# Optimization experiments

Measured on AMD Instinct MI355X. Metric: run time of the kernel, lower is better.

The kernel has to match this reference:

```python
import jax, jax.numpy as jnp
import numpy as np

B, N = 8, 512
EMBED, EDGE_D, FLAG_D = 256, 32, 32
NODE_NUM, EDGE_NUM, FLAG_NUM = 20000, 16, 4
IN_DIM = 2 * EMBED + 2 * FLAG_D + EDGE_D  # concat order: [head_emb, tail_emb, head_flag, tail_flag, edge]
NEG = -1e12


def setup_inputs() -> dict:
    key = jax.random.key(0)
    ks = jax.random.split(key, 16)
    s = 0.05
    return {
        "adjacent_matrix": jax.random.randint(ks[0], (B, N, N), 0, 2, dtype=jnp.int32),
        "head_nodes": jax.random.randint(ks[1], (B, N), 0, NODE_NUM, dtype=jnp.int32),
        "head_flag_bit_matrix": jax.random.randint(ks[2], (B, N), 0, FLAG_NUM, dtype=jnp.int32),
        "edge_type_matrix": jax.random.randint(ks[3], (B, N, N), 0, EDGE_NUM, dtype=jnp.int32),
        "node_emb": jax.random.normal(ks[4], (NODE_NUM, EMBED)) * s,
        "edge_emb": jax.random.normal(ks[5], (EDGE_NUM, EDGE_D)) * s,
        "flag_emb": jax.random.normal(ks[6], (FLAG_NUM, FLAG_D)) * s,
        "t1_w": jax.random.normal(ks[7], (EMBED, EMBED)) * s,
        "t1_b": jax.random.normal(ks[8], (EMBED,)) * s,
        "w1": jax.random.normal(ks[9], (IN_DIM,)) * s,
        "b1": jax.random.normal(ks[10], ()) * s,
        "t2_w": jax.random.normal(ks[11], (EMBED, EMBED)) * s,
        "t2_b": jax.random.normal(ks[12], (EMBED,)) * s,
        "w2": jax.random.normal(ks[13], (IN_DIM,)) * s,
        "b2": jax.random.normal(ks[14], ()) * s,
    }


def _leaky_relu(x):
    return jnp.where(x > 0, x, 0.1 * x)


def _gat_layer(h, f, e, adj, w, b):
    # Decompose Linear(concat([h_i, h_j, f_i, f_j, e_ij])) into per-part dot
    # products summed by broadcasting -> avoids the [B,N,N,IN_DIM] concat.
    D, F = h.shape[-1], f.shape[-1]
    wh, wt = w[:D], w[D:2 * D]
    wfh, wft = w[2 * D:2 * D + F], w[2 * D + F:2 * D + 2 * F]
    we = w[2 * D + 2 * F:]
    logit = ((h @ wh)[:, :, None] + (h @ wt)[:, None, :]
             + (f @ wfh)[:, :, None] + (f @ wft)[:, None, :]
             + jnp.einsum('bije,e->bij', e, we) + b)  # [B,N,N]
    logit = _leaky_relu(logit)
    logit = jnp.where(adj == 0, NEG, logit)
    att = jax.nn.softmax(logit, axis=1)  # softmax over head axis i
    # out[b,j] = sum_i att[b,i,j] * h[b,i]   (== bmm(att^T, h))
    return jnp.einsum('bij,bid->bjd', att, h)


def reference(adjacent_matrix, head_nodes, head_flag_bit_matrix, edge_type_matrix,
              node_emb, edge_emb, flag_emb,
              t1_w, t1_b, w1, b1, t2_w, t2_b, w2, b2):
    h = node_emb[head_nodes] @ t1_w.T + t1_b          # [B,N,D] (t1 projection)
    f = flag_emb[head_flag_bit_matrix]                # [B,N,F]
    e = edge_emb[edge_type_matrix]                    # [B,N,N,E]
    t = _gat_layer(h, f, e, adjacent_matrix, w1, b1)  # layer 1 aggregate
    t = jax.nn.sigmoid(t)
    h2 = t @ t2_w.T + t2_b                            # t2 projection
    return _gat_layer(h2, f, e, adjacent_matrix, w2, b2)
```

## Files before the change

### kernel.cpp

```cpp
#include <hip/hip_runtime.h>
#include <hip/hip_bf16.h>

#define BB 8
#define NN 512
#define DD 256
#define NROWS (BB*NN)
#define JT 16

using bf16x8 = __attribute__((ext_vector_type(8))) short;
using f32x4  = __attribute__((ext_vector_type(4))) float;
typedef unsigned short us_t;

__device__ __forceinline__ us_t f2bf(float x) {
    union { float f; unsigned int u; } v; v.f = x;
    unsigned int r = (v.u + 0x7fffu + ((v.u >> 16) & 1u)) >> 16;
    return (us_t)r;
}

__global__ __launch_bounds__(256) void prep_w(
    const float* __restrict__ w1f, const float* __restrict__ w2f,
    us_t* __restrict__ o1, us_t* __restrict__ o2)
{
    int i = blockIdx.x*1024 + threadIdx.x*4;
    float4 a = *(const float4*)(w1f + i);
    float4 b = *(const float4*)(w2f + i);
    ushort4 u;
    u.x = f2bf(a.x); u.y = f2bf(a.y); u.z = f2bf(a.z); u.w = f2bf(a.w);
    *(ushort4*)&o1[i] = u;
    u.x = f2bf(b.x); u.y = f2bf(b.y); u.z = f2bf(b.z); u.w = f2bf(b.w);
    *(ushort4*)&o2[i] = u;
}

__device__ __forceinline__ void lin_body(
    int bid, int t,
    const us_t* __restrict__ Wbf, const float* __restrict__ bias,
    const float* __restrict__ Xf, const int* __restrict__ idx,
    const float* __restrict__ wvec, const int* __restrict__ flagidx,
    const float* __restrict__ flag_emb,
    us_t* __restrict__ hT, float* __restrict__ aout, float* __restrict__ cout,
    float* redA, float* redC)
{
    const int wave = t >> 6, lane = t & 63;
    const int lrow = lane & 15, kg = lane >> 4;
    const int r0 = bid * 16;
    const int dw = wave * 64;

    const int arow = r0 + lrow;
    const int nid = idx ? idx[arow] : arow;

    f32x4 acc[4];
    #pragma unroll
    for (int n = 0; n < 4; ++n) acc[n] = (f32x4){0.f, 0.f, 0.f, 0.f};

    const float4* xr = (const float4*)(Xf + (size_t)nid * DD);
    #pragma unroll
    for (int ks = 0; ks < DD/32; ++ks) {
        float4 xa = xr[ks*8 + kg*2];
        float4 xb = xr[ks*8 + kg*2 + 1];
        bf16x8 af;
        af[0] = (short)f2bf(xa.x); af[1] = (short)f2bf(xa.y);
        af[2] = (short)f2bf(xa.z); af[3] = (short)f2bf(xa.w);
        af[4] = (short)f2bf(xb.x); af[5] = (short)f2bf(xb.y);
        af[6] = (short)f2bf(xb.z); af[7] = (short)f2bf(xb.w);
        #pragma unroll
        for (int n = 0; n < 4; ++n) {
            bf16x8 bfr = *(const bf16x8*)(Wbf + (size_t)(dw + n*16 + lrow)*DD
                                           + ks*32 + kg*8);
            acc[n] = __builtin_amdgcn_mfma_f32_16x16x32_bf16(af, bfr, acc[n], 0, 0, 0);
        }
    }

    const int b  = r0 >> 9;
    const int i0 = (r0 & 511) + kg*4;
    float pa[4] = {0.f,0.f,0.f,0.f}, pc[4] = {0.f,0.f,0.f,0.f};
    #pragma unroll
    for (int n = 0; n < 4; ++n) {
        int d = dw + n*16 + lrow;
        float bv = bias[d];
        float whd = wvec[d], wtd = wvec[256+d];
        ushort4 u;
        #pragma unroll
        for (int r = 0; r < 4; ++r) {
            float v = acc[n][r] + bv;
            ((us_t*)&u)[r] = f2bf(v);
            pa[r] += v * whd;
            pc[r] += v * wtd;
        }
        *(ushort4*)&hT[(size_t)b*DD*NN + (size_t)d*NN + i0] = u;
    }
    #pragma unroll
    for (int r = 0; r < 4; ++r) {
        #pragma unroll
        for (int m = 1; m < 16; m <<= 1) {
            pa[r] += __shfl_xor(pa[r], m);
            pc[r] += __shfl_xor(pc[r], m);
        }
    }
    if (lrow == 0) {
        #pragma unroll
        for (int r = 0; r < 4; ++r) {
            redA[wave*16 + kg*4 + r] = pa[r];
            redC[wave*16 + kg*4 + r] = pc[r];
        }
    }
    __syncthreads();
    if (t < 128) {
        const int m = t >> 3, sub = t & 7;
        const int fi = flagidx[r0 + m];
        float fa = 0.f, fc = 0.f;
        #pragma unroll
        for (int q = 0; q < 4; ++q) {
            int e = sub*4 + q;
            float fe = flag_emb[fi*32 + e];
            fa += fe * wvec[512 + e];
            fc += fe * wvec[544 + e];
        }
        #pragma unroll
        for (int mm = 1; mm < 8; mm <<= 1) {
            fa += __shfl_xor(fa, mm);
            fc += __shfl_xor(fc, mm);
        }
        if (sub == 0) {
            float sa = fa, sc = fc;
            #pragma unroll
            for (int wv = 0; wv < 4; ++wv) { sa += redA[wv*16 + m]; sc += redC[wv*16 + m]; }
            aout[r0 + m] = sa;
            cout[r0 + m] = sc;
        }
    }
}

__global__ __launch_bounds__(256) void k1(
    const us_t* __restrict__ Wb1, const float* __restrict__ bias1,
    const float* __restrict__ node_emb, const int* __restrict__ head_nodes,
    const float* __restrict__ wvec1, const int* __restrict__ flagidx,
    const float* __restrict__ flag_emb,
    us_t* __restrict__ hT, float* __restrict__ a1, float* __restrict__ c1,
    const int* __restrict__ adj, const int* __restrict__ et,
    unsigned char* __restrict__ pk)
{
    __shared__ float redA[64], redC[64];
    const int blk = blockIdx.x, t = threadIdx.x;
    if (blk < 256) {
        lin_body(blk, t, Wb1, bias1, node_emb, head_nodes,
                 wvec1, flagidx, flag_emb, hT, a1, c1, redA, redC);
    } else {
        int g = ((blk - 256)*256 + t)*4;
        int4 av = *(const int4*)(adj + g);
        int4 ev = *(const int4*)(et + g);
        uchar4 u;
        u.x = (unsigned char)((ev.x&15)|(av.x<<4));
        u.y = (unsigned char)((ev.y&15)|(av.y<<4));
        u.z = (unsigned char)((ev.z&15)|(av.z<<4));
        u.w = (unsigned char)((ev.w&15)|(av.w<<4));
        *(uchar4*)(pk + g) = u;
    }
}

__global__ __launch_bounds__(512) void attn1_lin2(
    const unsigned char* __restrict__ pk,
    const float* __restrict__ edge_emb, const float* __restrict__ w,
    const float* __restrict__ bptr,
    const float* __restrict__ a, const float* __restrict__ c,
    const us_t* __restrict__ hT,
    const us_t* __restrict__ Wb2, const float* __restrict__ bias2,
    const float* __restrict__ wvec2, const int* __restrict__ flagidx,
    const float* __restrict__ flag_emb,
    us_t* __restrict__ hT2, float* __restrict__ a2, float* __restrict__ c2)
{
    __shared__ __align__(16) float p[NN][JT+1];
    __shared__ __align__(16) us_t Pb[JT][NN+8];
    __shared__ __align__(16) us_t Sg[16][DD+8];
    __shared__ float as[NN];
    __shared__ float edot[16];
    __shared__ float cjs[JT];
    __shared__ float red[32][JT];
    __shared__ float mj[JT];
    __shared__ float invden[JT];

    float* redA = &red[0][0];
    float* redC = &red[8][0];

    const int t = threadIdx.x;
    const int b  = blockIdx.x >> 5;
    const int j0 = (blockIdx.x & 31) * JT;

    as[t & 511] = a[b*NN + (t & 511)];
    if (t < 16) {
        float s = 0.f;
        for (int e2 = 0; e2 < 32; ++e2)
            s += edge_emb[t*32 + e2] * w[576 + e2];
        edot[t] = s;
    } else if (t < 32) {
        cjs[t-16] = c[b*NN + j0 + (t-16)];
    }
    const float bias = bptr[0];
    __syncthreads();

    const unsigned char* pkb = pk + (size_t)b*NN*NN + j0;
    #pragma unroll
    for (int it = 0; it < 4; ++it) {
        int lid4 = (it*512 + t) * 4;
        int i = lid4 >> 4, jj = lid4 & 15;
        uchar4 u = *(const uchar4*)(pkb + (size_t)i*NN + jj);
        float base = as[i] + bias;
        unsigned char uv[4] = {u.x, u.y, u.z, u.w};
        #pragma unroll
        for (int q = 0; q < 4; ++q) {
            float l = base + cjs[jj+q] + edot[uv[q] & 15];
            l = (l > 0.f) ? l : 0.1f*l;
            p[i][jj+q] = (uv[q] >> 4) ? l : -1.0e30f;
        }
    }
    __syncthreads();

    const int j = t & 15, grp = t >> 4;
    float m = -3.0e38f;
    #pragma unroll
    for (int s = 0; s < 16; ++s) m = fmaxf(m, p[grp + s*32][j]);
    red[grp][j] = m;
    __syncthreads();
    if (t < 16) {
        float mm = red[0][t];
        for (int g2 = 1; g2 < 32; ++g2) mm = fmaxf(mm, red[g2][t]);
        mj[t] = mm;
    }
    __syncthreads();
    const float mmax = mj[j];
    float ssum = 0.f;
    #pragma unroll
    for (int s = 0; s < 16; ++s) {
        float v = __expf(p[grp + s*32][j] - mmax);
        p[grp + s*32][j] = v;
        ssum += v;
    }
    red[grp][j] = ssum;
    __syncthreads();
    if (t < 16) {
        float sm = 0.f;
        for (int g2 = 0; g2 < 32; ++g2) sm += red[g2][t];
        invden[t] = 1.f / sm;
    }
    __syncthreads();

    const float inv = invden[j];
    #pragma unroll
    for (int s = 0; s < 8; ++s) {
        int i = grp*2 + s*64;
        ushort2 u;
        u.x = f2bf(p[i  ][j] * inv);
        u.y = f2bf(p[i+1][j] * inv);
        *(ushort2*)&Pb[j][i] = u;
    }
    __syncthreads();

    const int wave = t >> 6, lane = t & 63;
    const int dw = wave * 32;
    const int lrow = lane & 15;
    const int kg   = lane >> 4;
    f32x4 acc[2];
    acc[0] = (f32x4){0.f,0.f,0.f,0.f};
    acc[1] = (f32x4){0.f,0.f,0.f,0.f};

    const us_t* hTb = hT + (size_t)b*DD*NN;
    const us_t* hp[2];
    hp[0] = hTb + (size_t)(dw + lrow)*NN + kg*8;
    hp[1] = hTb + (size_t)(dw + 16 + lrow)*NN + kg*8;

    #pragma unroll 4
    for (int ks = 0; ks < NN/32; ++ks) {
        int k0 = ks*32;
        bf16x8 afr = *(const bf16x8*)&Pb[lrow][kg*8 + k0];
        #pragma unroll
        for (int n = 0; n < 2; ++n) {
            bf16x8 bfr = *(const bf16x8*)(hp[n] + k0);
            acc[n] = __builtin_amdgcn_mfma_f32_16x16x32_bf16(afr, bfr, acc[n], 0, 0, 0);
        }
    }

    #pragma unroll
    for (int n = 0; n < 2; ++n) {
        #pragma unroll
        for (int r = 0; r < 4; ++r) {
            float v = 1.f/(1.f + __expf(-acc[n][r]));
            Sg[kg*4 + r][dw + n*16 + lrow] = f2bf(v);
        }
    }
    __syncthreads();

    f32x4 acc2[2];
    acc2[0] = (f32x4){0.f,0.f,0.f,0.f};
    acc2[1] = (f32x4){0.f,0.f,0.f,0.f};
    #pragma unroll
    for (int ks = 0; ks < DD/32; ++ks) {
        bf16x8 af2 = *(const bf16x8*)&Sg[lrow][ks*32 + kg*8];
        #pragma unroll
        for (int n = 0; n < 2; ++n) {
            bf16x8 bf2 = *(const bf16x8*)(Wb2 + (size_t)(dw + n*16 + lrow)*DD
                                           + ks*32 + kg*8);
            acc2[n] = __builtin_amdgcn_mfma_f32_16x16x32_bf16(af2, bf2, acc2[n], 0, 0, 0);
        }
    }

    const int r0 = b*NN + j0;
    const int i0 = j0 + kg*4;
    float pa[4] = {0.f,0.f,0.f,0.f}, pc[4] = {0.f,0.f,0.f,0.f};
    #pragma unroll
    for (int n = 0; n < 2; ++n) {
        int d = dw + n*16 + lrow;
        float bv = bias2[d];
        float whd = wvec2[d], wtd = wvec2[256+d];
        ushort4 u;
        #pragma unroll
        for (int r = 0; r < 4; ++r) {
            float v = acc2[n][r] + bv;
            ((us_t*)&u)[r] = f2bf(v);
            pa[r] += v * whd;
            pc[r] += v * wtd;
        }
        *(ushort4*)&hT2[(size_t)b*DD*NN + (size_t)d*NN + i0] = u;
    }
    #pragma unroll
    for (int r = 0; r < 4; ++r) {
        #pragma unroll
        for (int mk = 1; mk < 16; mk <<= 1) {
            pa[r] += __shfl_xor(pa[r], mk);
            pc[r] += __shfl_xor(pc[r], mk);
        }
    }
    __syncthreads();
    if (lrow == 0) {
        #pragma unroll
        for (int r = 0; r < 4; ++r) {
            redA[wave*16 + kg*4 + r] = pa[r];
            redC[wave*16 + kg*4 + r] = pc[r];
        }
    }
    __syncthreads();
    if (t < 128) {
        const int mrow = t >> 3, sub = t & 7;
        const int fi = flagidx[r0 + mrow];
        float fa = 0.f, fc = 0.f;
        #pragma unroll
        for (int q = 0; q < 4; ++q) {
            int e = sub*4 + q;
            float fe = flag_emb[fi*32 + e];
            fa += fe * wvec2[512 + e];
            fc += fe * wvec2[544 + e];
        }
        #pragma unroll
        for (int mm = 1; mm < 8; mm <<= 1) {
            fa += __shfl_xor(fa, mm);
            fc += __shfl_xor(fc, mm);
        }
        if (sub == 0) {
            float sa = fa, sc = fc;
            #pragma unroll
            for (int wv = 0; wv < 8; ++wv) { sa += redA[wv*16 + mrow]; sc += redC[wv*16 + mrow]; }
            a2[r0 + mrow] = sa;
            c2[r0 + mrow] = sc;
        }
    }
}

__global__ __launch_bounds__(512) void attn2(
    const unsigned char* __restrict__ pk,
    const float* __restrict__ edge_emb, const float* __restrict__ w,
    const float* __restrict__ bptr,
    const float* __restrict__ a, const float* __restrict__ c,
    const us_t* __restrict__ hT,
    float* __restrict__ outf)
{
    __shared__ __align__(16) float p[NN][JT+1];
    __shared__ __align__(16) us_t Pb[JT][NN+8];
    __shared__ float as[NN];
    __shared__ float edot[16];
    __shared__ float cjs[JT];
    __shared__ float red[32][JT];
    __shared__ float mj[JT];
    __shared__ float invden[JT];

    const int t = threadIdx.x;
    const int b  = blockIdx.x >> 5;
    const int j0 = (blockIdx.x & 31) * JT;

    as[t & 511] = a[b*NN + (t & 511)];
    if (t < 16) {
        float s = 0.f;
        for (int e2 = 0; e2 < 32; ++e2)
            s += edge_emb[t*32 + e2] * w[576 + e2];
        edot[t] = s;
    } else if (t < 32) {
        cjs[t-16] = c[b*NN + j0 + (t-16)];
    }
    const float bias = bptr[0];
    __syncthreads();

    const unsigned char* pkb = pk + (size_t)b*NN*NN + j0;
    #pragma unroll
    for (int it = 0; it < 4; ++it) {
        int lid4 = (it*512 + t) * 4;
        int i = lid4 >> 4, jj = lid4 & 15;
        uchar4 u = *(const uchar4*)(pkb + (size_t)i*NN + jj);
        float base = as[i] + bias;
        unsigned char uv[4] = {u.x, u.y, u.z, u.w};
        #pragma unroll
        for (int q = 0; q < 4; ++q) {
            float l = base + cjs[jj+q] + edot[uv[q] & 15];
            l = (l > 0.f) ? l : 0.1f*l;
            p[i][jj+q] = (uv[q] >> 4) ? l : -1.0e30f;
        }
    }
    __syncthreads();

    const int j = t & 15, grp = t >> 4;
    float m = -3.0e38f;
    #pragma unroll
    for (int s = 0; s < 16; ++s) m = fmaxf(m, p[grp + s*32][j]);
    red[grp][j] = m;
    __syncthreads();
    if (t < 16) {
        float mm = red[0][t];
        for (int g2 = 1; g2 < 32; ++g2) mm = fmaxf(mm, red[g2][t]);
        mj[t] = mm;
    }
    __syncthreads();
    const float mmax = mj[j];
    float ssum = 0.f;
    #pragma unroll
    for (int s = 0; s < 16; ++s) {
        float v = __expf(p[grp + s*32][j] - mmax);
        p[grp + s*32][j] = v;
        ssum += v;
    }
    red[grp][j] = ssum;
    __syncthreads();
    if (t < 16) {
        float sm = 0.f;
        for (int g2 = 0; g2 < 32; ++g2) sm += red[g2][t];
        invden[t] = 1.f / sm;
    }
    __syncthreads();

    const float inv = invden[j];
    #pragma unroll
    for (int s = 0; s < 8; ++s) {
        int i = grp*2 + s*64;
        ushort2 u;
        u.x = f2bf(p[i  ][j] * inv);
        u.y = f2bf(p[i+1][j] * inv);
        *(ushort2*)&Pb[j][i] = u;
    }
    __syncthreads();

    const int wave = t >> 6, lane = t & 63;
    const int dw = wave * 32;
    const int lrow = lane & 15;
    const int kg   = lane >> 4;
    f32x4 acc[2];
    acc[0] = (f32x4){0.f,0.f,0.f,0.f};
    acc[1] = (f32x4){0.f,0.f,0.f,0.f};

    const us_t* hTb = hT + (size_t)b*DD*NN;
    const us_t* hp[2];
    hp[0] = hTb + (size_t)(dw + lrow)*NN + kg*8;
    hp[1] = hTb + (size_t)(dw + 16 + lrow)*NN + kg*8;

    #pragma unroll 4
    for (int ks = 0; ks < NN/32; ++ks) {
        int k0 = ks*32;
        bf16x8 afr = *(const bf16x8*)&Pb[lrow][kg*8 + k0];
        #pragma unroll
        for (int n = 0; n < 2; ++n) {
            bf16x8 bfr = *(const bf16x8*)(hp[n] + k0);
            acc[n] = __builtin_amdgcn_mfma_f32_16x16x32_bf16(afr, bfr, acc[n], 0, 0, 0);
        }
    }

    #pragma unroll
    for (int n = 0; n < 2; ++n) {
        #pragma unroll
        for (int r = 0; r < 4; ++r) {
            int jj = j0 + kg*4 + r;
            int dd = dw + n*16 + lrow;
            outf[(size_t)(b*NN + jj)*DD + dd] = acc[n][r];
        }
    }
}

extern "C" void kernel_launch(void* const* d_in, const int* in_sizes, int n_in,
                              void* d_out, int out_size, void* d_ws, size_t ws_size,
                              hipStream_t stream) {
    (void)in_sizes; (void)n_in; (void)out_size; (void)ws_size;
    const int*   adj       = (const int*)d_in[0];
    const int*   head_nodes= (const int*)d_in[1];
    const int*   head_flag = (const int*)d_in[2];
    const int*   etype     = (const int*)d_in[3];
    const float* node_emb  = (const float*)d_in[4];
    const float* edge_emb  = (const float*)d_in[5];
    const float* flag_emb  = (const float*)d_in[6];
    const float* t1_w      = (const float*)d_in[7];
    const float* t1_b      = (const float*)d_in[8];
    const float* w1        = (const float*)d_in[9];
    const float* b1        = (const float*)d_in[10];
    const float* t2_w      = (const float*)d_in[11];
    const float* t2_b      = (const float*)d_in[12];
    const float* w2        = (const float*)d_in[13];
    const float* b2        = (const float*)d_in[14];

    us_t* hT1 = (us_t*)d_ws;
    us_t* hT2 = hT1 + (size_t)NROWS*DD;
    us_t* Wb1 = hT2 + (size_t)NROWS*DD;
    us_t* Wb2 = Wb1 + (size_t)DD*DD;
    unsigned char* pk = (unsigned char*)(Wb2 + (size_t)DD*DD);
    float* a1 = (float*)(pk + (size_t)BB*NN*NN);
    float* c1 = a1 + NROWS;
    float* a2 = c1 + NROWS;
    float* c2 = a2 + NROWS;

    prep_w<<<DD*DD/1024, 256, 0, stream>>>(t1_w, t2_w, Wb1, Wb2);
    k1<<<256 + BB*NN*NN/1024, 256, 0, stream>>>(
        Wb1, t1_b, node_emb, head_nodes, w1, head_flag, flag_emb,
        hT1, a1, c1, adj, etype, pk);
    attn1_lin2<<<BB*(NN/JT), 512, 0, stream>>>(
        pk, edge_emb, w1, b1, a1, c1, hT1,
        Wb2, t2_b, w2, head_flag, flag_emb, hT2, a2, c2);
    attn2<<<BB*(NN/JT), 512, 0, stream>>>(
        pk, edge_emb, w2, b2, a2, c2, hT2, (float*)d_out);
}
```

Measured before the change: 54.00 us.

## Drop packed adjacency/edge buffer and prep_w kernel; read raw int inputs in attention

Removes the packing pass that combined adj and edge types into one byte per pair. Both attention kernels now read the int32 adj and etype arrays directly. The separate prep_w launch is also removed: t1_w is converted to bf16 inline inside k1's MFMA loop, and t2_w conversion moves into extra blocks of k1. This saves one launch and the pack write and read, but each attention kernel now reads 8 bytes per pair instead of 1, doubling raw int traffic across the two layers, and k1 repeats the weight conversion in every block.

```diff
diff --git a/kernel.cpp b/kernel.cpp
--- a/kernel.cpp
+++ b/kernel.cpp
@@ -17,42 +17,39 @@
     return (us_t)r;
 }
 
-__global__ __launch_bounds__(256) void prep_w(
-    const float* __restrict__ w1f, const float* __restrict__ w2f,
-    us_t* __restrict__ o1, us_t* __restrict__ o2)
+__global__ __launch_bounds__(256) void k1(
+    const float* __restrict__ w1f, const float* __restrict__ bias1,
+    const float* __restrict__ node_emb, const int* __restrict__ head_nodes,
+    const float* __restrict__ wvec1, const int* __restrict__ flagidx,
+    const float* __restrict__ flag_emb,
+    us_t* __restrict__ hT, float* __restrict__ a1, float* __restrict__ c1,
+    const float* __restrict__ w2f, us_t* __restrict__ Wb2)
 {
-    int i = blockIdx.x*1024 + threadIdx.x*4;
-    float4 a = *(const float4*)(w1f + i);
-    float4 b = *(const float4*)(w2f + i);
-    ushort4 u;
-    u.x = f2bf(a.x); u.y = f2bf(a.y); u.z = f2bf(a.z); u.w = f2bf(a.w);
-    *(ushort4*)&o1[i] = u;
-    u.x = f2bf(b.x); u.y = f2bf(b.y); u.z = f2bf(b.z); u.w = f2bf(b.w);
-    *(ushort4*)&o2[i] = u;
-}
-
-__device__ __forceinline__ void lin_body(
-    int bid, int t,
-    const us_t* __restrict__ Wbf, const float* __restrict__ bias,
-    const float* __restrict__ Xf, const int* __restrict__ idx,
-    const float* __restrict__ wvec, const int* __restrict__ flagidx,
-    const float* __restrict__ flag_emb,
-    us_t* __restrict__ hT, float* __restrict__ aout, float* __restrict__ cout,
-    float* redA, float* redC)
-{
+    __shared__ float redA[64], redC[64];
+    const int blk = blockIdx.x, t = threadIdx.x;
+
+    if (blk >= 256) {
+        int i = (blk - 256)*1024 + t*4;
+        float4 wv = *(const float4*)(w2f + i);
+        ushort4 u;
+        u.x = f2bf(wv.x); u.y = f2bf(wv.y); u.z = f2bf(wv.z); u.w = f2bf(wv.w);
+        *(ushort4*)&Wb2[i] = u;
+        return;
+    }
+
     const int wave = t >> 6, lane = t & 63;
     const int lrow = lane & 15, kg = lane >> 4;
-    const int r0 = bid * 16;
+    const int r0 = blk * 16;
     const int dw = wave * 64;
 
     const int arow = r0 + lrow;
-    const int nid = idx ? idx[arow] : arow;
+    const int nid = head_nodes[arow];
 
     f32x4 acc[4];
     #pragma unroll
     for (int n = 0; n < 4; ++n) acc[n] = (f32x4){0.f, 0.f, 0.f, 0.f};
 
-    const float4* xr = (const float4*)(Xf + (size_t)nid * DD);
+    const float4* xr = (const float4*)(node_emb + (size_t)nid * DD);
     #pragma unroll
     for (int ks = 0; ks < DD/32; ++ks) {
         float4 xa = xr[ks*8 + kg*2];
@@ -64,8 +61,14 @@
         af[6] = (short)f2bf(xb.z); af[7] = (short)f2bf(xb.w);
         #pragma unroll
         for (int n = 0; n < 4; ++n) {
-            bf16x8 bfr = *(const bf16x8*)(Wbf + (size_t)(dw + n*16 + lrow)*DD
-                                           + ks*32 + kg*8);
+            const float4* wr = (const float4*)(w1f + (size_t)(dw + n*16 + lrow)*DD
+                                                + ks*32 + kg*8);
+            float4 wa = wr[0], wb = wr[1];
+            bf16x8 bfr;
+            bfr[0] = (short)f2bf(wa.x); bfr[1] = (short)f2bf(wa.y);
+            bfr[2] = (short)f2bf(wa.z); bfr[3] = (short)f2bf(wa.w);
+            bfr[4] = (short)f2bf(wb.x); bfr[5] = (short)f2bf(wb.y);
+            bfr[6] = (short)f2bf(wb.z); bfr[7] = (short)f2bf(wb.w);
             acc[n] = __builtin_amdgcn_mfma_f32_16x16x32_bf16(af, bfr, acc[n], 0, 0, 0);
         }
     }
@@ -76,8 +79,8 @@
     #pragma unroll
     for (int n = 0; n < 4; ++n) {
         int d = dw + n*16 + lrow;
-        float bv = bias[d];
-        float whd = wvec[d], wtd = wvec[256+d];
+        float bv = bias1[d];
+        float whd = wvec1[d], wtd = wvec1[256+d];
         ushort4 u;
         #pragma unroll
         for (int r = 0; r < 4; ++r) {
@@ -112,8 +115,8 @@
         for (int q = 0; q < 4; ++q) {
             int e = sub*4 + q;
             float fe = flag_emb[fi*32 + e];
-            fa += fe * wvec[512 + e];
-            fc += fe * wvec[544 + e];
+            fa += fe * wvec1[512 + e];
+            fc += fe * wvec1[544 + e];
         }
         #pragma unroll
         for (int mm = 1; mm < 8; mm <<= 1) {
@@ -124,41 +127,40 @@
             float sa = fa, sc = fc;
             #pragma unroll
             for (int wv = 0; wv < 4; ++wv) { sa += redA[wv*16 + m]; sc += redC[wv*16 + m]; }
-            aout[r0 + m] = sa;
-            cout[r0 + m] = sc;
+            a1[r0 + m] = sa;
+            c1[r0 + m] = sc;
         }
     }
 }
 
-__global__ __launch_bounds__(256) void k1(
-    const us_t* __restrict__ Wb1, const float* __restrict__ bias1,
-    const float* __restrict__ node_emb, const int* __restrict__ head_nodes,
-    const float* __restrict__ wvec1, const int* __restrict__ flagidx,
-    const float* __restrict__ flag_emb,
-    us_t* __restrict__ hT, float* __restrict__ a1, float* __restrict__ c1,
-    const int* __restrict__ adj, const int* __restrict__ et,
-    unsigned char* __restrict__ pk)
+__device__ __forceinline__ void logits_raw(
+    int t, int b, int j0,
+    const int* __restrict__ adj, const int* __restrict__ etype,
+    const float* as, const float* cjs, const float* edot, float bias,
+    float (*p)[JT+1])
 {
-    __shared__ float redA[64], redC[64];
-    const int blk = blockIdx.x, t = threadIdx.x;
-    if (blk < 256) {
-        lin_body(blk, t, Wb1, bias1, node_emb, head_nodes,
-                 wvec1, flagidx, flag_emb, hT, a1, c1, redA, redC);
-    } else {
-        int g = ((blk - 256)*256 + t)*4;
+    const int base = (b*NN)*NN + j0;
+    #pragma unroll
+    for (int it = 0; it < 4; ++it) {
+        int lid4 = (it*512 + t) * 4;
+        int i = lid4 >> 4, jj = lid4 & 15;
+        const int g = base + i*NN + jj;
         int4 av = *(const int4*)(adj + g);
-        int4 ev = *(const int4*)(et + g);
-        uchar4 u;
-        u.x = (unsigned char)((ev.x&15)|(av.x<<4));
-        u.y = (unsigned char)((ev.y&15)|(av.y<<4));
-        u.z = (unsigned char)((ev.z&15)|(av.z<<4));
-        u.w = (unsigned char)((ev.w&15)|(av.w<<4));
-        *(uchar4*)(pk + g) = u;
+        int4 ev = *(const int4*)(etype + g);
+        float bse = as[i] + bias;
+        int avv[4] = {av.x, av.y, av.z, av.w};
+        int evv[4] = {ev.x, ev.y, ev.z, ev.w};
+        #pragma unroll
+        for (int q = 0; q < 4; ++q) {
+            float l = bse + cjs[jj+q] + edot[evv[q]];
+            l = (l > 0.f) ? l : 0.1f*l;
+            p[i][jj+q] = avv[q] ? l : -1.0e30f;
+        }
     }
 }
 
 __global__ __launch_bounds__(512) void attn1_lin2(
-    const unsigned char* __restrict__ pk,
+    const int* __restrict__ adj, const int* __restrict__ etype,
     const float* __restrict__ edge_emb, const float* __restrict__ w,
     const float* __restrict__ bptr,
     const float* __restrict__ a, const float* __restrict__ c,
@@ -197,21 +199,7 @@
     const float bias = bptr[0];
     __syncthreads();
 
-    const unsigned char* pkb = pk + (size_t)b*NN*NN + j0;
-    #pragma unroll
-    for (int it = 0; it < 4; ++it) {
-        int lid4 = (it*512 + t) * 4;
-        int i = lid4 >> 4, jj = lid4 & 15;
-        uchar4 u = *(const uchar4*)(pkb + (size_t)i*NN + jj);
-        float base = as[i] + bias;
-        unsigned char uv[4] = {u.x, u.y, u.z, u.w};
-        #pragma unroll
-        for (int q = 0; q < 4; ++q) {
-            float l = base + cjs[jj+q] + edot[uv[q] & 15];
-            l = (l > 0.f) ? l : 0.1f*l;
-            p[i][jj+q] = (uv[q] >> 4) ? l : -1.0e30f;
-        }
-    }
+    logits_raw(t, b, j0, adj, etype, as, cjs, edot, bias, p);
     __syncthreads();
 
     const int j = t & 15, grp = t >> 4;
@@ -364,7 +352,7 @@
 }
 
 __global__ __launch_bounds__(512) void attn2(
-    const unsigned char* __restrict__ pk,
+    const int* __restrict__ adj, const int* __restrict__ etype,
     const float* __restrict__ edge_emb, const float* __restrict__ w,
     const float* __restrict__ bptr,
     const float* __restrict__ a, const float* __restrict__ c,
@@ -396,21 +384,7 @@
     const float bias = bptr[0];
     __syncthreads();
 
-    const unsigned char* pkb = pk + (size_t)b*NN*NN + j0;
-    #pragma unroll
-    for (int it = 0; it < 4; ++it) {
-        int lid4 = (it*512 + t) * 4;
-        int i = lid4 >> 4, jj = lid4 & 15;
-        uchar4 u = *(const uchar4*)(pkb + (size_t)i*NN + jj);
-        float base = as[i] + bias;
-        unsigned char uv[4] = {u.x, u.y, u.z, u.w};
-        #pragma unroll
-        for (int q = 0; q < 4; ++q) {
-            float l = base + cjs[jj+q] + edot[uv[q] & 15];
-            l = (l > 0.f) ? l : 0.1f*l;
-            p[i][jj+q] = (uv[q] >> 4) ? l : -1.0e30f;
-        }
-    }
+    logits_raw(t, b, j0, adj, etype, as, cjs, edot, bias, p);
     __syncthreads();
 
     const int j = t & 15, grp = t >> 4;
@@ -510,21 +484,18 @@
 
     us_t* hT1 = (us_t*)d_ws;
     us_t* hT2 = hT1 + (size_t)NROWS*DD;
-    us_t* Wb1 = hT2 + (size_t)NROWS*DD;
-    us_t* Wb2 = Wb1 + (size_t)DD*DD;
-    unsigned char* pk = (unsigned char*)(Wb2 + (size_t)DD*DD);
-    float* a1 = (float*)(pk + (size_t)BB*NN*NN);
+    us_t* Wb2 = hT2 + (size_t)NROWS*DD;
+    float* a1 = (float*)(Wb2 + (size_t)DD*DD);
     float* c1 = a1 + NROWS;
     float* a2 = c1 + NROWS;
     float* c2 = a2 + NROWS;
 
-    prep_w<<<DD*DD/1024, 256, 0, stream>>>(t1_w, t2_w, Wb1, Wb2);
-    k1<<<256 + BB*NN*NN/1024, 256, 0, stream>>>(
-        Wb1, t1_b, node_emb, head_nodes, w1, head_flag, flag_emb,
-        hT1, a1, c1, adj, etype, pk);
+    k1<<<320, 256, 0, stream>>>(
+        t1_w, t1_b, node_emb, head_nodes, w1, head_flag, flag_emb,
+        hT1, a1, c1, t2_w, Wb2);
     attn1_lin2<<<BB*(NN/JT), 512, 0, stream>>>(
-        pk, edge_emb, w1, b1, a1, c1, hT1,
+        adj, etype, edge_emb, w1, b1, a1, c1, hT1,
         Wb2, t2_b, w2, head_flag, flag_emb, hT2, a2, c2);
     attn2<<<BB*(NN/JT), 512, 0, stream>>>(
-        pk, edge_emb, w2, b2, a2, c2, hT2, (float*)d_out);
+        adj, etype, edge_emb, w2, b2, a2, c2, hT2, (float*)d_out);
 }
```

After: 55.98 us. 3.7% more time.
